# Performance work log

Measured on AMD Instinct MI355X. Metric: run time of the kernel, lower is better.

The kernel has to match this reference:

```python
import jax, jax.numpy as jnp
import numpy as np

B = 32768
F = 256
H1 = 16
H2 = 8

def setup_inputs() -> dict:
    key = jax.random.key(0)
    ks = jax.random.split(key, 9)
    x = jax.random.normal(ks[0], (B, F), dtype=jnp.float32)
    # Stacked per-feature MLP params (one UnivariateNetwork per feature)
    W1 = jax.random.normal(ks[1], (F, H1), dtype=jnp.float32) * (1.0 / np.sqrt(1))
    b1 = jax.random.normal(ks[2], (F, H1), dtype=jnp.float32) * 0.05
    W2 = jax.random.normal(ks[3], (F, H1, H2), dtype=jnp.float32) * (1.0 / np.sqrt(H1))
    b2 = jax.random.normal(ks[4], (F, H2), dtype=jnp.float32) * 0.05
    W3 = jax.random.normal(ks[5], (F, H2), dtype=jnp.float32) * (1.0 / np.sqrt(H2))
    b3 = jax.random.normal(ks[6], (F,), dtype=jnp.float32) * 0.05
    theta = jax.random.uniform(ks[7], (F,), dtype=jnp.float32) * 0.05
    bias = jnp.zeros((1,), dtype=jnp.float32)
    return {"x": x, "W1": W1, "b1": b1, "W2": W2, "b2": b2,
            "W3": W3, "b3": b3, "theta": theta, "bias": bias}

def reference(x, W1, b1, W2, b2, W3, b3, theta, bias):
    # Batched per-feature MLP: 1 -> H1 -> H2 -> 1 with ELU, all features at once.
    h1 = jax.nn.elu(x[:, :, None] * W1[None, :, :] + b1[None, :, :])      # [B, F, H1]
    h2 = jax.nn.elu(jnp.einsum('bfh,fhk->bfk', h1, W2) + b2[None, :, :])  # [B, F, H2]
    Z = jnp.einsum('bfk,fk->bf', h2, W3) + b3[None, :]                    # [B, F]
    weights = jax.nn.softplus(theta)                                      # [F]
    y_pred = Z @ weights + bias                                           # [B]
    return (y_pred, weights, Z)
```

## Files before the change

kernel.cpp:

```cpp
#include <hip/hip_runtime.h>

#define NB 32768
#define NF 256
#define H1 16
#define H2 8
#define ROWS_PER_BLOCK 1024
#define ITERS (ROWS_PER_BLOCK / 64)
#define FPB 4
#define NT (FPB * 64)

__device__ __forceinline__ float elu_f(float v) {
    return v > 0.0f ? v : (__expf(v) - 1.0f);
}
__device__ __forceinline__ float rfl(float v) {
    return __int_as_float(__builtin_amdgcn_readfirstlane(__float_as_int(v)));
}

__global__ __launch_bounds__(NT, 5)
void z_kernel(const float* __restrict__ x,  const float* __restrict__ W1,
              const float* __restrict__ b1, const float* __restrict__ W2,
              const float* __restrict__ b2, const float* __restrict__ W3,
              const float* __restrict__ b3, float* __restrict__ z_out) {
    const int wave = threadIdx.x >> 6;
    const int lane = threadIdx.x & 63;
    const int f    = blockIdx.y * FPB + wave;
    const int rowBase = blockIdx.x * ROWS_PER_BLOCK;

    __shared__ float lds_w2[FPB][32];

    if (lane < 8) {
        const float4 v = reinterpret_cast<const float4*>(W2 + f * H1 * H2 + 64)[lane];
        reinterpret_cast<float4*>(lds_w2[wave])[lane] = v;
    }

    float s_w2[8 * H2];
    {
        const float4* p = reinterpret_cast<const float4*>(W2 + f * H1 * H2);
        #pragma unroll
        for (int i = 0; i < 16; ++i) {
            float4 v = p[i];
            s_w2[4*i]   = rfl(v.x); s_w2[4*i+1] = rfl(v.y);
            s_w2[4*i+2] = rfl(v.z); s_w2[4*i+3] = rfl(v.w);
        }
    }
    float w2v[32];
    {
        const float4* p = reinterpret_cast<const float4*>(W2 + f * H1 * H2 + 96);
        #pragma unroll
        for (int i = 0; i < 8; ++i) {
            float4 v = p[i];
            w2v[4*i]=v.x; w2v[4*i+1]=v.y; w2v[4*i+2]=v.z; w2v[4*i+3]=v.w;
        }
    }
    float w1v[H1], s_b1[H1];
    {
        const float4* pw = reinterpret_cast<const float4*>(W1 + f * H1);
        const float4* pb = reinterpret_cast<const float4*>(b1 + f * H1);
        #pragma unroll
        for (int i = 0; i < 4; ++i) {
            float4 v = pw[i];
            w1v[4*i] = v.x; w1v[4*i+1] = v.y; w1v[4*i+2] = v.z; w1v[4*i+3] = v.w;
        }
        #pragma unroll
        for (int i = 0; i < 4; ++i) {
            float4 v = pb[i];
            s_b1[4*i]   = rfl(v.x); s_b1[4*i+1] = rfl(v.y);
            s_b1[4*i+2] = rfl(v.z); s_b1[4*i+3] = rfl(v.w);
        }
    }
    float b2v[H2];
    {
        const float4* p = reinterpret_cast<const float4*>(b2 + f * H2);
        float4 v0 = p[0], v1 = p[1];
        b2v[0]=v0.x; b2v[1]=v0.y; b2v[2]=v0.z; b2v[3]=v0.w;
        b2v[4]=v1.x; b2v[5]=v1.y; b2v[6]=v1.z; b2v[7]=v1.w;
    }
    float s_w3[H2];
    {
        const float4* p = reinterpret_cast<const float4*>(W3 + f * H2);
        float4 v0 = p[0], v1 = p[1];
        s_w3[0]=rfl(v0.x); s_w3[1]=rfl(v0.y); s_w3[2]=rfl(v0.z); s_w3[3]=rfl(v0.w);
        s_w3[4]=rfl(v1.x); s_w3[5]=rfl(v1.y); s_w3[6]=rfl(v1.z); s_w3[7]=rfl(v1.w);
    }
    const float s_b3 = rfl(b3[f]);

    __syncthreads();

    const float* wbase = lds_w2[wave];

    int off = (rowBase + lane) * NF + f;
    float xv = x[off];
    float xn = x[off + 64 * NF];

    #pragma unroll 1
    for (int it = 0; it < ITERS; ++it) {
        const int off2 = off + 2 * 64 * NF;
        const float xnn = x[(it + 2 < ITERS) ? off2 : off];

        float acc[H2];
        #pragma unroll
        for (int k = 0; k < H2; ++k) acc[k] = b2v[k];

        #pragma unroll
        for (int h = 0; h < 8; ++h) {
            const float h1 = elu_f(fmaf(xv, w1v[h], s_b1[h]));
            #pragma unroll
            for (int k = 0; k < H2; ++k)
                acc[k] = fmaf(h1, s_w2[h * H2 + k], acc[k]);
        }

        int dsoff = 0;
        asm volatile("" : "+v"(dsoff));
        const float4* wp = reinterpret_cast<const float4*>(wbase + dsoff);
        #pragma unroll
        for (int h = 0; h < 4; ++h) {
            const float4 wlo = wp[2 * h];
            const float4 whi = wp[2 * h + 1];
            const float h1 = elu_f(fmaf(xv, w1v[8 + h], s_b1[8 + h]));
            acc[0] = fmaf(h1, wlo.x, acc[0]);
            acc[1] = fmaf(h1, wlo.y, acc[1]);
            acc[2] = fmaf(h1, wlo.z, acc[2]);
            acc[3] = fmaf(h1, wlo.w, acc[3]);
            acc[4] = fmaf(h1, whi.x, acc[4]);
            acc[5] = fmaf(h1, whi.y, acc[5]);
            acc[6] = fmaf(h1, whi.z, acc[6]);
            acc[7] = fmaf(h1, whi.w, acc[7]);
        }

        #pragma unroll
        for (int h = 0; h < 4; ++h) {
            const float h1 = elu_f(fmaf(xv, w1v[12 + h], s_b1[12 + h]));
            #pragma unroll
            for (int k = 0; k < H2; ++k)
                acc[k] = fmaf(h1, w2v[h * H2 + k], acc[k]);
        }

        float z = s_b3;
        #pragma unroll
        for (int k = 0; k < H2; ++k)
            z = fmaf(elu_f(acc[k]), s_w3[k], z);

        z_out[off] = z;
        off += 64 * NF; xv = xn; xn = xnn;
    }
}

#define NT2 256
#define ROWS2 64
__global__ __launch_bounds__(NT2, 4)
void y_kernel(const float* __restrict__ z, const float* __restrict__ theta,
              const float* __restrict__ bias, float* __restrict__ y_out,
              float* __restrict__ w_out) {
    __shared__ __align__(16) float wls[NF];
    const int tid = threadIdx.x;
    {
        const float th = theta[tid];
        const float w  = logf(1.0f + __expf(th));
        wls[tid] = w;
        if (blockIdx.x == 0) w_out[tid] = w;
    }
    __syncthreads();
    const int wave = tid >> 6, lane = tid & 63;
    const float4 w4 = reinterpret_cast<const float4*>(wls)[lane];
    const float biasv = bias[0];
    #pragma unroll 1
    for (int r = 0; r < ROWS2 / 4; ++r) {
        const int row = blockIdx.x * ROWS2 + wave * (ROWS2 / 4) + r;
        const float4 zv = reinterpret_cast<const float4*>(z + row * NF)[lane];
        float s = zv.x * w4.x + zv.y * w4.y + zv.z * w4.z + zv.w * w4.w;
        #pragma unroll
        for (int o = 32; o > 0; o >>= 1) s += __shfl_down(s, o, 64);
        if (lane == 0) y_out[row] = s + biasv;
    }
}

extern "C" void kernel_launch(void* const* d_in, const int* in_sizes, int n_in,
                              void* d_out, int out_size, void* d_ws, size_t ws_size,
                              hipStream_t stream) {
    const float* x     = (const float*)d_in[0];
    const float* W1    = (const float*)d_in[1];
    const float* b1    = (const float*)d_in[2];
    const float* W2    = (const float*)d_in[3];
    const float* b2    = (const float*)d_in[4];
    const float* W3    = (const float*)d_in[5];
    const float* b3    = (const float*)d_in[6];
    const float* theta = (const float*)d_in[7];
    const float* bias  = (const float*)d_in[8];

    float* y_out = (float*)d_out;
    float* w_out = y_out + NB;
    float* z_out = w_out + NF;

    dim3 grid1(NB / ROWS_PER_BLOCK, NF / FPB);
    z_kernel<<<grid1, NT, 0, stream>>>(x, W1, b1, W2, b2, W3, b3, z_out);
    y_kernel<<<NB / ROWS2, NT2, 0, stream>>>(z_out, theta, bias, y_out, w_out);
}
```

Before: 161.3 us.

## Stage x loads and z stores through LDS as float4 per row

Each wave used to read and write one scalar per row at stride NF, so a single access touched only 4 bytes per 1 KB row. Now 16 lanes per wave load a float4 covering the block's 4 features per row into a double-buffered LDS tile. Z values are gathered into LDS and written back as float4. The aim is fewer, wider global transactions, at the cost of one __syncthreads per iteration and only 16 of 64 lanes doing I/O. Prefetch distance also drops from two iterations to one.

```diff
diff --git a/kernel.cpp b/kernel.cpp
--- a/kernel.cpp
+++ b/kernel.cpp
@@ -23,10 +23,13 @@
               const float* __restrict__ b3, float* __restrict__ z_out) {
     const int wave = threadIdx.x >> 6;
     const int lane = threadIdx.x & 63;
-    const int f    = blockIdx.y * FPB + wave;
+    const int f0   = blockIdx.y * FPB;
+    const int f    = f0 + wave;
     const int rowBase = blockIdx.x * ROWS_PER_BLOCK;
 
     __shared__ float lds_w2[FPB][32];
+    __shared__ float xbuf[2][FPB][64];
+    __shared__ float zbuf[2][64][5];
 
     if (lane < 8) {
         const float4 v = reinterpret_cast<const float4*>(W2 + f * H1 * H2 + 64)[lane];
@@ -84,18 +87,30 @@
     }
     const float s_b3 = rfl(b3[f]);
 
+    const int r16 = (lane & 15);
+    const bool io = (lane < 16);
+    const int myrow = wave * 16 + r16;
+    if (io) {
+        const float4 v = *reinterpret_cast<const float4*>(
+            x + (size_t)(rowBase + myrow) * NF + f0);
+        xbuf[0][0][myrow] = v.x; xbuf[0][1][myrow] = v.y;
+        xbuf[0][2][myrow] = v.z; xbuf[0][3][myrow] = v.w;
+    }
     __syncthreads();
 
     const float* wbase = lds_w2[wave];
-
-    int off = (rowBase + lane) * NF + f;
-    float xv = x[off];
-    float xn = x[off + 64 * NF];
+    int cur = 0;
 
     #pragma unroll 1
     for (int it = 0; it < ITERS; ++it) {
-        const int off2 = off + 2 * 64 * NF;
-        const float xnn = x[(it + 2 < ITERS) ? off2 : off];
+        float4 xnext;
+        if (io) {
+            const int nit = (it + 1 < ITERS) ? it + 1 : it;
+            xnext = *reinterpret_cast<const float4*>(
+                x + (size_t)(rowBase + nit * 64 + myrow) * NF + f0);
+        }
+
+        const float xv = xbuf[cur][wave][lane];
 
         float acc[H2];
         #pragma unroll
@@ -140,8 +155,23 @@
         for (int k = 0; k < H2; ++k)
             z = fmaf(elu_f(acc[k]), s_w3[k], z);
 
-        z_out[off] = z;
-        off += 64 * NF; xv = xn; xn = xnn;
+        zbuf[cur][lane][wave] = z;
+
+        if (io) {
+            xbuf[cur ^ 1][0][myrow] = xnext.x; xbuf[cur ^ 1][1][myrow] = xnext.y;
+            xbuf[cur ^ 1][2][myrow] = xnext.z; xbuf[cur ^ 1][3][myrow] = xnext.w;
+        }
+
+        __syncthreads();
+
+        if (io) {
+            float4 zq;
+            zq.x = zbuf[cur][myrow][0]; zq.y = zbuf[cur][myrow][1];
+            zq.z = zbuf[cur][myrow][2]; zq.w = zbuf[cur][myrow][3];
+            *reinterpret_cast<float4*>(
+                z_out + (size_t)(rowBase + it * 64 + myrow) * NF + f0) = zq;
+        }
+        cur ^= 1;
     }
 }
 
```

Result: slower. 169.4 us (+5.1%).
